# Kernel tuning notes

Measured on AMD Instinct MI355X. Metric: run time of the kernel, lower is better.

The kernel has to match this reference:

```python
import jax, jax.numpy as jnp
import numpy as np
from jax import lax

RATIOS = [0.5, 1.0, 2.0]
SCALES = [8, 16, 32]
BASE = 16
FEAT_STRIDE = 16
NMS_THRESH = 0.7
PRE_NMS = 2000
POST_NMS = 300
MIN_SIZE = 16.0
SCALE = 1.0
A = len(RATIOS) * len(SCALES)  # 9


def _anchor_base():
    ab = []
    py = px = BASE / 2.0
    for r in RATIOS:
        for s in SCALES:
            h = BASE * s * np.sqrt(r)
            w = BASE * s * np.sqrt(1.0 / r)
            ab.append([py - h / 2.0, px - w / 2.0, py + h / 2.0, px + w / 2.0])
    return jnp.asarray(np.array(ab, dtype=np.float32))  # (A,4)


def _shifted_anchors(H, W):
    base = _anchor_base()
    sy = jnp.arange(H, dtype=jnp.float32) * FEAT_STRIDE
    sx = jnp.arange(W, dtype=jnp.float32) * FEAT_STRIDE
    gy, gx = jnp.meshgrid(sy, sx, indexing='ij')
    shift = jnp.stack([gy.ravel(), gx.ravel(), gy.ravel(), gx.ravel()], axis=1)  # (K,4)
    return (shift[:, None, :] + base[None, :, :]).reshape(-1, 4)  # (K*A,4)


def _conv(x, w, b, pad):
    y = lax.conv_general_dilated(x, w, (1, 1), ((pad, pad), (pad, pad)),
                                 dimension_numbers=('NCHW', 'OIHW', 'NCHW'))
    return y + b[None, :, None, None]


def _loc2bbox(anchor, loc):
    h = anchor[:, 2] - anchor[:, 0]
    w = anchor[:, 3] - anchor[:, 1]
    cy = anchor[:, 0] + 0.5 * h
    cx = anchor[:, 1] + 0.5 * w
    dy, dx, dh, dw = loc[:, 0], loc[:, 1], loc[:, 2], loc[:, 3]
    ncy = dy * h + cy
    ncx = dx * w + cx
    nh = jnp.exp(dh) * h
    nw = jnp.exp(dw) * w
    return jnp.stack([ncy - 0.5 * nh, ncx - 0.5 * nw, ncy + 0.5 * nh, ncx + 0.5 * nw], axis=1)


def _iou_matrix(b):
    area = (b[:, 2] - b[:, 0]) * (b[:, 3] - b[:, 1])
    ty = jnp.maximum(b[:, None, 0], b[None, :, 0])
    tx = jnp.maximum(b[:, None, 1], b[None, :, 1])
    by = jnp.minimum(b[:, None, 2], b[None, :, 2])
    bx = jnp.minimum(b[:, None, 3], b[None, :, 3])
    inter = jnp.maximum(by - ty, 0.0) * jnp.maximum(bx - tx, 0.0)
    return inter / (area[:, None] + area[None, :] - inter)


def _proposals(loc_i, fg_i, anchor, img_h, img_w):
    boxes = _loc2bbox(anchor, loc_i)
    boxes = jnp.stack([
        jnp.clip(boxes[:, 0], 0.0, float(img_h)),
        jnp.clip(boxes[:, 1], 0.0, float(img_w)),
        jnp.clip(boxes[:, 2], 0.0, float(img_h)),
        jnp.clip(boxes[:, 3], 0.0, float(img_w)),
    ], axis=1)
    hs = boxes[:, 2] - boxes[:, 0]
    ws = boxes[:, 3] - boxes[:, 1]
    valid = (hs >= MIN_SIZE * SCALE) & (ws >= MIN_SIZE * SCALE)
    sc = jnp.where(valid, fg_i, -jnp.inf)
    top_sc, idx = lax.top_k(sc, PRE_NMS)          # sorted by score desc
    b = boxes[idx]                                # (PRE_NMS,4)
    iou = _iou_matrix(b)                          # (PRE_NMS,PRE_NMS)
    rng = jnp.arange(PRE_NMS)

    def body(i, keep):
        sup = (iou[i] > NMS_THRESH) & keep[i] & (rng > i)
        return keep & ~sup

    keep = lax.fori_loop(0, PRE_NMS, body, top_sc > -jnp.inf)
    order = jnp.argsort(jnp.where(keep, rng, PRE_NMS))  # kept indices first, score order
    sel = order[:POST_NMS]
    n_keep = jnp.sum(keep)
    valid_out = jnp.arange(POST_NMS) < n_keep
    rois = jnp.where(valid_out[:, None], b[sel], 0.0)
    return rois, valid_out


def setup_inputs() -> dict:
    key = jax.random.key(0)
    ks = jax.random.split(key, 4)
    return {
        'x': jax.random.normal(ks[0], (4, 1024, 64, 64), dtype=jnp.float32),
        'conv1_w': 0.01 * jax.random.normal(ks[1], (512, 1024, 3, 3), dtype=jnp.float32),
        'conv1_b': jnp.zeros((512,), dtype=jnp.float32),
        'score_w': 0.01 * jax.random.normal(ks[2], (18, 512, 1, 1), dtype=jnp.float32),
        'score_b': jnp.zeros((18,), dtype=jnp.float32),
        'loc_w': 0.01 * jax.random.normal(ks[3], (36, 512, 1, 1), dtype=jnp.float32),
        'loc_b': jnp.zeros((36,), dtype=jnp.float32),
        'img_h': 1024,
        'img_w': 1024,
    }


def reference(x, conv1_w, conv1_b, score_w, score_b, loc_w, loc_b, img_h, img_w):
    n, _, H, W = x.shape
    anchor = _shifted_anchors(H, W)                       # (HWA,4)
    mid = jax.nn.relu(_conv(x, conv1_w, conv1_b, 1))
    rpn_locs = _conv(mid, loc_w, loc_b, 0).transpose(0, 2, 3, 1).reshape(n, -1, 4)
    rpn_scores = _conv(mid, score_w, score_b, 0).transpose(0, 2, 3, 1)
    soft = jax.nn.softmax(rpn_scores.reshape(n, H, W, A, 2), axis=4)
    rpn_fg = soft[..., 1].reshape(n, -1)
    rpn_scores = rpn_scores.reshape(n, -1, 2)
    rois, valid = jax.vmap(lambda l, s: _proposals(l, s, anchor, img_h, img_w))(rpn_locs, rpn_fg)
    roi_indices = jnp.where(valid, jnp.arange(n, dtype=jnp.int32)[:, None], -1)
    return (rpn_locs, rpn_scores, rois.reshape(-1, 4), roi_indices.reshape(-1), anchor)
```

## Files before the change

### kernel.cpp

```cpp
#include <hip/hip_runtime.h>
#include <math.h>

#define NIMG 4
#define CIN 1024
#define CMID 512
#define HGT 64
#define WID 64
#define NA 9
#define NPOS 36864
#define PRE 2000
#define POST 300

#define LOCOFF   0
#define SCOREOFF 589824
#define ROISOFF  884736
#define RIDXOFF  889536
#define ANCHOFF  890736

__global__ __launch_bounds__(256) void wtrans_kernel(
    const float* __restrict__ w, float* __restrict__ wt)
{
    __shared__ float ts[64][65];
    const int t = threadIdx.x;
    const int rt0 = blockIdx.x * 64;
    const int ct0 = blockIdx.y * 64;
    const int j = t & 63;
    const int i0 = t >> 6;
#pragma unroll
    for (int k = 0; k < 16; ++k) {
        int i = i0 + k * 4;
        ts[i][j] = w[(size_t)(ct0 + i) * (CIN * 9) + rt0 + j];
    }
    __syncthreads();
#pragma unroll
    for (int k = 0; k < 16; ++k) {
        int jj = i0 + k * 4;
        wt[(size_t)(rt0 + jj) * CMID + ct0 + j] = ts[j][jj];
    }
}

__global__ __launch_bounds__(256) void conv1_kernel(
    const float* __restrict__ x, const float* __restrict__ wt,
    const float* __restrict__ bias, float* __restrict__ mid)
{
    __shared__ __align__(16) float  xs[8][6][68];
    __shared__ __align__(16) double wsh[8][9][32];
    const int t = threadIdx.x;
    const int rowgrp = blockIdx.x, coutgrp = blockIdx.y, img = blockIdx.z;
    const int r0 = rowgrp * 4, c0 = coutgrp * 32;
    const int pixgrp = t & 7, cgrp = (t >> 3) & 7, rowi = t >> 6;
    const int p0 = pixgrp * 8, cc0 = cgrp * 4;

    double acc[8][4];
#pragma unroll
    for (int i = 0; i < 8; ++i)
#pragma unroll
        for (int c = 0; c < 4; ++c) acc[i][c] = 0.0;

    for (int ci0 = 0; ci0 < CIN; ci0 += 8) {
        for (int idx = t; idx < 8 * 6 * 66; idx += 256) {
            int cin = idx / 396, rem = idx % 396;
            int row = rem / 66, col = rem % 66;
            int gr = r0 - 1 + row, gc = col - 1;
            float v = 0.f;
            if (gr >= 0 && gr < HGT && gc >= 0 && gc < WID)
                v = x[((img * CIN + ci0 + cin) * HGT + gr) * WID + gc];
            xs[cin][row][col] = v;
        }
        for (int idx = t; idx < 8 * 9 * 32; idx += 256) {
            int cout = idx & 31, r = idx >> 5;
            wsh[r / 9][r % 9][cout] =
                (double)wt[(size_t)((ci0 + r / 9) * 9 + r % 9) * CMID + c0 + cout];
        }
        __syncthreads();

#pragma unroll 1
        for (int cin = 0; cin < 8; ++cin) {
#pragma unroll
            for (int dy = 0; dy < 3; ++dy) {
                const float* xr = &xs[cin][rowi + dy][p0];
                float4 xa = *(const float4*)xr;
                float4 xb = *(const float4*)(xr + 4);
                float2 xc = *(const float2*)(xr + 8);
                double xd[10];
                xd[0] = (double)xa.x; xd[1] = (double)xa.y;
                xd[2] = (double)xa.z; xd[3] = (double)xa.w;
                xd[4] = (double)xb.x; xd[5] = (double)xb.y;
                xd[6] = (double)xb.z; xd[7] = (double)xb.w;
                xd[8] = (double)xc.x; xd[9] = (double)xc.y;
#pragma unroll
                for (int dx = 0; dx < 3; ++dx) {
                    const double* wp = &wsh[cin][dy * 3 + dx][cc0];
                    double2 wa = *(const double2*)(wp);
                    double2 wb = *(const double2*)(wp + 2);
                    double w0 = wa.x, w1 = wa.y, w2 = wb.x, w3 = wb.y;
#pragma unroll
                    for (int i = 0; i < 8; ++i) {
                        double xv = xd[i + dx];
                        acc[i][0] += xv * w0;
                        acc[i][1] += xv * w1;
                        acc[i][2] += xv * w2;
                        acc[i][3] += xv * w3;
                    }
                }
            }
        }
        __syncthreads();
    }

#pragma unroll
    for (int co = 0; co < 4; ++co) {
        double bb = (double)bias[c0 + cc0 + co];
        float tmp[8];
#pragma unroll
        for (int i = 0; i < 8; ++i) {
            double v = acc[i][co] + bb;
            v = v > 0.0 ? v : 0.0;
            tmp[i] = (float)v;
        }
        float* dst = &mid[((img * CMID + c0 + cc0 + co) * HGT + (r0 + rowi)) * WID + p0];
        *(float4*)dst = make_float4(tmp[0], tmp[1], tmp[2], tmp[3]);
        *(float4*)(dst + 4) = make_float4(tmp[4], tmp[5], tmp[6], tmp[7]);
    }
}

__global__ __launch_bounds__(256) void conv1x1_kernel(
    const float* __restrict__ mid,
    const float* __restrict__ sw, const float* __restrict__ sb,
    const float* __restrict__ lw, const float* __restrict__ lb,
    float* __restrict__ out, double* __restrict__ locws, double* __restrict__ keyws)
{
    const int t = threadIdx.x;
    const int p = blockIdx.x * 256 + t;
    const int g = blockIdx.y;
    const int img = blockIdx.z;

    double acc[14];
#pragma unroll
    for (int k = 0; k < 14; ++k) acc[k] = 0.0;

    const float* mp = &mid[(size_t)img * CMID * 4096 + p];
    for (int cin = 0; cin < CMID; ++cin) {
        double xd = (double)mp[(size_t)cin * 4096];
#pragma unroll
        for (int k = 0; k < 14; ++k) {
            int c = g * 14 + k;
            double wv = 0.0;
            if (c < 36)      wv = (double)lw[c * CMID + cin];
            else if (c < 54) wv = (double)sw[(c - 36) * CMID + cin];
            acc[k] += xd * wv;
        }
    }

    double prev = 0.0;
#pragma unroll
    for (int k = 0; k < 14; ++k) {
        int c = g * 14 + k;
        if (c >= 54) continue;
        if (c < 36) {
            double v = acc[k] + (double)lb[c];
            int a = c >> 2, cc = c & 3;
            size_t ix = (size_t)img * NPOS + (size_t)p * NA + a;
            locws[ix * 4 + cc] = v;
            out[LOCOFF + ix * 4 + cc] = (float)v;
        } else {
            int sc = c - 36;
            double v = acc[k] + (double)sb[sc];
            int a = sc >> 1;
            size_t ix = (size_t)img * NPOS + (size_t)p * NA + a;
            out[SCOREOFF + ix * 2 + (sc & 1)] = (float)v;
            if (sc & 1) keyws[ix] = v - prev;
            prev = v;
        }
    }
}

__device__ __forceinline__ unsigned mono_of(double k) {
    unsigned fb = __float_as_uint((float)k);
    return (fb & 0x80000000u) ? ~fb : (fb | 0x80000000u);
}

__global__ __launch_bounds__(256) void boxes_kernel(
    double* __restrict__ keyio, const double* __restrict__ locws,
    const int* __restrict__ imh, const int* __restrict__ imw,
    float* __restrict__ out, double* __restrict__ boxes, unsigned* __restrict__ hist)
{
    __shared__ unsigned lh[4096];
    const int t = threadIdx.x;
    const int img = blockIdx.y;
    const int pos = blockIdx.x * 256 + t;
    for (int i = t; i < 4096; i += 256) lh[i] = 0;
    __syncthreads();

    int a = pos % 9, hw = pos / 9;
    int hy = hw >> 6, hx = hw & 63;
    int r_idx = a / 3, s_idx = a % 3;
    double ratio = r_idx == 0 ? 0.5 : (r_idx == 1 ? 1.0 : 2.0);
    double scl   = s_idx == 0 ? 8.0 : (s_idx == 1 ? 16.0 : 32.0);
    double hh2 = 8.0 * scl * sqrt(ratio);
    double ww2 = 8.0 * scl * sqrt(1.0 / ratio);
    float ay1 = (float)(8.0 - hh2), ax1 = (float)(8.0 - ww2);
    float ay2 = (float)(8.0 + hh2), ax2 = (float)(8.0 + ww2);
    float sy = (float)(hy * 16), sx = (float)(hx * 16);
    float A0 = sy + ay1, A1 = sx + ax1, A2 = sy + ay2, A3 = sx + ax2;
    if (img == 0) {
        size_t ao = ANCHOFF + (size_t)pos * 4;
        out[ao + 0] = A0; out[ao + 1] = A1; out[ao + 2] = A2; out[ao + 3] = A3;
    }

    size_t ix = (size_t)img * NPOS + pos;
    const double* lp = &locws[ix * 4];
    double h = (double)A2 - (double)A0, w_ = (double)A3 - (double)A1;
    double cy = (double)A0 + 0.5 * h, cx = (double)A1 + 0.5 * w_;
    double dy = lp[0], dx = lp[1], dh = lp[2], dw = lp[3];
    double ncy = dy * h + cy, ncx = dx * w_ + cx;
    double nh = exp(dh) * h, nw = exp(dw) * w_;
    double Hc = (double)imh[0], Wc = (double)imw[0];
    double y1 = ncy - 0.5 * nh, x1 = ncx - 0.5 * nw;
    double y2 = ncy + 0.5 * nh, x2 = ncx + 0.5 * nw;
    y1 = fmin(fmax(y1, 0.0), Hc); x1 = fmin(fmax(x1, 0.0), Wc);
    y2 = fmin(fmax(y2, 0.0), Hc); x2 = fmin(fmax(x2, 0.0), Wc);
    boxes[ix * 4 + 0] = y1; boxes[ix * 4 + 1] = x1;
    boxes[ix * 4 + 2] = y2; boxes[ix * 4 + 3] = x2;

    bool valid = ((y2 - y1) >= 16.0) && ((x2 - x1) >= 16.0);
    double kg = valid ? keyio[ix] : -INFINITY;
    keyio[ix] = kg;
    atomicAdd(&lh[mono_of(kg) >> 20], 1u);
    __syncthreads();
    for (int i = t; i < 4096; i += 256)
        if (lh[i]) atomicAdd(&hist[img * 4096 + i], lh[i]);
}

__global__ void cutoff_kernel(const unsigned* __restrict__ hist, int* __restrict__ cutoffb)
{
    if (threadIdx.x) return;
    int img = blockIdx.x;
    unsigned cum = 0; int cb = 0;
    for (int b = 4095; b >= 0; --b) {
        cum += hist[img * 4096 + b];
        if (cum >= PRE) { cb = b; break; }
    }
    cutoffb[img] = cb;
}

__global__ __launch_bounds__(256) void compact_kernel(
    const double* __restrict__ keyio, const int* __restrict__ cutoffb,
    int* __restrict__ candCnt, int* __restrict__ candIdx, double* __restrict__ candKey)
{
    int img = blockIdx.y;
    int pos = blockIdx.x * 256 + threadIdx.x;
    size_t ix = (size_t)img * NPOS + pos;
    double k = keyio[ix];
    if ((int)(mono_of(k) >> 20) >= cutoffb[img]) {
        int p = atomicAdd(&candCnt[img], 1);
        candIdx[img * NPOS + p] = pos;
        candKey[(size_t)img * NPOS + p] = k;
    }
}

__global__ __launch_bounds__(256) void rank_kernel(
    const int* __restrict__ candCnt, const int* __restrict__ candIdx,
    const double* __restrict__ candKey, const double* __restrict__ boxes,
    int* __restrict__ topIdx, int* __restrict__ topValid, double* __restrict__ bsel)
{
    __shared__ double sk[256];
    __shared__ int si[256];
    int img = blockIdx.y, t = threadIdx.x;
    int M = candCnt[img];
    if (blockIdx.x * 256 >= M) return;
    int i = blockIdx.x * 256 + t;
    bool act = i < M;
    double ki = 0.0; int pi = 0;
    if (act) { ki = candKey[(size_t)img * NPOS + i]; pi = candIdx[img * NPOS + i]; }
    int rank = 0;
    for (int jb = 0; jb < M; jb += 256) {
        int j = jb + t;
        if (j < M) { sk[t] = candKey[(size_t)img * NPOS + j]; si[t] = candIdx[img * NPOS + j]; }
        __syncthreads();
        int lim = min(256, M - jb);
        if (act) {
            for (int jj = 0; jj < lim; ++jj) {
                double kj = sk[jj]; int pj = si[jj];
                rank += (kj > ki || (kj == ki && pj < pi)) ? 1 : 0;
            }
        }
        __syncthreads();
    }
    if (act && rank < PRE) {
        topIdx[img * PRE + rank] = pi;
        topValid[img * PRE + rank] = (ki != -INFINITY) ? 1 : 0;
        const double* bp = &boxes[((size_t)img * NPOS + pi) * 4];
        double* bs = &bsel[((size_t)img * PRE + rank) * 4];
        bs[0] = bp[0]; bs[1] = bp[1]; bs[2] = bp[2]; bs[3] = bp[3];
    }
}

__global__ __launch_bounds__(256) void mask_kernel(
    const double* __restrict__ bsel, unsigned long long* __restrict__ mask)
{
    int i = blockIdx.x, img = blockIdx.y, t = threadIdx.x;
    const double* bi = &bsel[((size_t)img * PRE + i) * 4];
    double y1i = bi[0], x1i = bi[1], y2i = bi[2], x2i = bi[3];
    double ai = (y2i - y1i) * (x2i - x1i);
#pragma unroll 1
    for (int it = 0; it < 8; ++it) {
        int j = it * 256 + t;
        bool pred = false;
        if (j < PRE && j > i) {
            const double* bj = &bsel[((size_t)img * PRE + j) * 4];
            double ty = fmax(y1i, bj[0]), tx = fmax(x1i, bj[1]);
            double by = fmin(y2i, bj[2]), bx = fmin(x2i, bj[3]);
            double inter = fmax(by - ty, 0.0) * fmax(bx - tx, 0.0);
            double aj = (bj[2] - bj[0]) * (bj[3] - bj[1]);
            double iou = inter / (ai + aj - inter);
            pred = iou > 0.7;
        }
        unsigned long long m = __ballot(pred);
        if ((t & 63) == 0)
            mask[((size_t)img * PRE + i) * 32 + it * 4 + (t >> 6)] = m;
    }
}

__global__ void nms_kernel(const unsigned long long* __restrict__ mask,
                           const int* __restrict__ topValid, int* __restrict__ keepA)
{
    int img = blockIdx.x, lane = threadIdx.x;
    size_t base = (size_t)img * PRE;
    unsigned long long remv = 0;
    if (lane < 32) {
        unsigned long long tv = 0;
        for (int b = 0; b < 64; ++b) {
            int idx = lane * 64 + b;
            if (idx < PRE && topValid[base + idx]) tv |= (1ull << b);
        }
        remv = ~tv;
    }
    const unsigned long long* mrow = &mask[base * 32];
    unsigned long long c0 = 0, c1 = 0, c2 = 0, c3 = 0;
    if (lane < 32) {
        c0 = mrow[(size_t)0 * 32 + lane]; c1 = mrow[(size_t)1 * 32 + lane];
        c2 = mrow[(size_t)2 * 32 + lane]; c3 = mrow[(size_t)3 * 32 + lane];
    }
    for (int i = 0; i < PRE; i += 4) {
        unsigned long long n0 = 0, n1 = 0, n2 = 0, n3 = 0;
        if (lane < 32 && i + 4 < PRE) {
            n0 = mrow[(size_t)(i + 4) * 32 + lane];
            n1 = mrow[(size_t)(i + 5) * 32 + lane];
            n2 = mrow[(size_t)(i + 6) * 32 + lane];
            n3 = mrow[(size_t)(i + 7) * 32 + lane];
        }
        {
            unsigned long long rw = __shfl(remv, i >> 6);
            int kp = !((rw >> (i & 63)) & 1ull);
            if (lane == 0) keepA[base + i] = kp;
            if (kp) remv |= c0;
        }
        {
            int ii = i + 1;
            unsigned long long rw = __shfl(remv, ii >> 6);
            int kp = !((rw >> (ii & 63)) & 1ull);
            if (lane == 0) keepA[base + ii] = kp;
            if (kp) remv |= c1;
        }
        {
            int ii = i + 2;
            unsigned long long rw = __shfl(remv, ii >> 6);
            int kp = !((rw >> (ii & 63)) & 1ull);
            if (lane == 0) keepA[base + ii] = kp;
            if (kp) remv |= c2;
        }
        {
            int ii = i + 3;
            unsigned long long rw = __shfl(remv, ii >> 6);
            int kp = !((rw >> (ii & 63)) & 1ull);
            if (lane == 0) keepA[base + ii] = kp;
            if (kp) remv |= c3;
        }
        c0 = n0; c1 = n1; c2 = n2; c3 = n3;
    }
}

__global__ __launch_bounds__(256) void final_kernel(
    const int* __restrict__ keepA, const double* __restrict__ bsel, float* __restrict__ out)
{
    __shared__ int ssum[256];
    __shared__ int stot;
    int img = blockIdx.x, t = threadIdx.x;
    size_t base = (size_t)img * PRE;
    int loc[8]; int s = 0;
#pragma unroll
    for (int k = 0; k < 8; ++k) {
        int i = t * 8 + k;
        loc[k] = (i < PRE) ? keepA[base + i] : 0;
        s += loc[k];
    }
    ssum[t] = s;
    __syncthreads();
    if (t == 0) {
        int run = 0;
        for (int u = 0; u < 256; ++u) { int tmp = ssum[u]; ssum[u] = run; run += tmp; }
        stot = run;
    }
    __syncthreads();
    int run = ssum[t];
#pragma unroll
    for (int k = 0; k < 8; ++k) {
        int i = t * 8 + k;
        if (i < PRE && loc[k]) {
            int p = run++;
            if (p < POST) {
                const double* bp = &bsel[(base + i) * 4];
                size_t ro = ROISOFF + ((size_t)img * POST + p) * 4;
                out[ro + 0] = (float)bp[0]; out[ro + 1] = (float)bp[1];
                out[ro + 2] = (float)bp[2]; out[ro + 3] = (float)bp[3];
                out[RIDXOFF + img * POST + p] = (float)img;
            }
        }
    }
    __syncthreads();
    int nk = stot;
    for (int r = t; r < POST; r += 256) {
        if (r >= nk) {
            size_t ro = ROISOFF + ((size_t)img * POST + r) * 4;
            out[ro + 0] = 0.f; out[ro + 1] = 0.f; out[ro + 2] = 0.f; out[ro + 3] = 0.f;
            out[RIDXOFF + img * POST + r] = -1.f;
        }
    }
}

extern "C" void kernel_launch(void* const* d_in, const int* in_sizes, int n_in,
                              void* d_out, int out_size, void* d_ws, size_t ws_size,
                              hipStream_t stream)
{
    const float* x   = (const float*)d_in[0];
    const float* c1w = (const float*)d_in[1];
    const float* c1b = (const float*)d_in[2];
    const float* sw  = (const float*)d_in[3];
    const float* sb  = (const float*)d_in[4];
    const float* lw  = (const float*)d_in[5];
    const float* lb  = (const float*)d_in[6];
    const int*   ih  = (const int*)d_in[7];
    const int*   iw  = (const int*)d_in[8];
    float* out = (float*)d_out;
    (void)in_sizes; (void)n_in; (void)out_size; (void)ws_size;

    char* ws = (char*)d_ws;
    size_t off = 0;
    auto alloc = [&](size_t bytes) -> void* {
        void* p = (void*)(ws + off);
        off = (off + bytes + 255) & ~(size_t)255;
        return p;
    };
    float*  mid      = (float*) alloc((size_t)NIMG * CMID * 4096 * 4);
    float*  wtr      = (float*) alloc((size_t)CMID * CIN * 9 * 4);
    double* locws    = (double*)alloc((size_t)NIMG * NPOS * 4 * 8);
    double* keyws    = (double*)alloc((size_t)NIMG * NPOS * 8);
    double* boxes    = (double*)alloc((size_t)NIMG * NPOS * 4 * 8);
    unsigned* hist   = (unsigned*)alloc((size_t)NIMG * 4096 * 4);
    int*    cutoffb  = (int*)   alloc(64);
    int*    candCnt  = (int*)   alloc(64);
    int*    candIdx  = (int*)   alloc((size_t)NIMG * NPOS * 4);
    double* candKey  = (double*)alloc((size_t)NIMG * NPOS * 8);
    int*    topIdx   = (int*)   alloc((size_t)NIMG * PRE * 4);
    int*    topValid = (int*)   alloc((size_t)NIMG * PRE * 4);
    double* bsel     = (double*)alloc((size_t)NIMG * PRE * 4 * 8);
    unsigned long long* mask = (unsigned long long*)alloc((size_t)NIMG * PRE * 32 * 8);
    int*    keepA    = (int*)   alloc((size_t)NIMG * PRE * 4);

    hipMemsetAsync(hist, 0, (size_t)NIMG * 4096 * 4, stream);
    hipMemsetAsync(candCnt, 0, 64, stream);

    wtrans_kernel <<<dim3(144, 8),       256, 0, stream>>>(c1w, wtr);
    conv1_kernel  <<<dim3(16, 16, NIMG), 256, 0, stream>>>(x, wtr, c1b, mid);
    conv1x1_kernel<<<dim3(16, 4, NIMG),  256, 0, stream>>>(mid, sw, sb, lw, lb, out, locws, keyws);
    boxes_kernel  <<<dim3(144, NIMG),    256, 0, stream>>>(keyws, locws, ih, iw, out, boxes, hist);
    cutoff_kernel <<<NIMG, 64, 0, stream>>>(hist, cutoffb);
    compact_kernel<<<dim3(144, NIMG),    256, 0, stream>>>(keyws, cutoffb, candCnt, candIdx, candKey);
    rank_kernel   <<<dim3(144, NIMG),    256, 0, stream>>>(candCnt, candIdx, candKey, boxes,
                                                           topIdx, topValid, bsel);
    mask_kernel   <<<dim3(PRE, NIMG),    256, 0, stream>>>(bsel, mask);
    nms_kernel    <<<NIMG, 64, 0, stream>>>(mask, topValid, keepA);
    final_kernel  <<<NIMG, 256, 0, stream>>>(keepA, bsel, out);
}
```

Before: 4.658 ms.

## Double-buffer conv1 loads via direct global-to-LDS with pre-converted fp64 weight slabs

The 3x3 conv now stages input rows and weights straight into LDS with global_load_lds, double-buffered so the next channel block loads while the current one computes. Only one barrier per iteration remains. Weights are pre-converted to double and laid out in contiguous per-cout-group slabs so they can be copied without conversion. Horizontal padding is handled in registers instead of being stored as halo columns. The cost is twice the weight workspace, a smaller channel block per stage, and correctness depends on the async LDS load semantics and the buffer-reuse ordering.

```diff
diff --git a/kernel.cpp b/kernel.cpp
--- a/kernel.cpp
+++ b/kernel.cpp
@@ -10,6 +10,7 @@
 #define NPOS 36864
 #define PRE 2000
 #define POST 300
+#define CBLK 4
 
 #define LOCOFF   0
 #define SCOREOFF 589824
@@ -17,8 +18,11 @@
 #define RIDXOFF  889536
 #define ANCHOFF  890736
 
+typedef __attribute__((address_space(1))) const void glob_cv;
+typedef __attribute__((address_space(3))) void lds_v;
+
 __global__ __launch_bounds__(256) void wtrans_kernel(
-    const float* __restrict__ w, float* __restrict__ wt)
+    const float* __restrict__ w, double* __restrict__ wt64)
 {
     __shared__ float ts[64][65];
     const int t = threadIdx.x;
@@ -32,24 +36,64 @@
         ts[i][j] = w[(size_t)(ct0 + i) * (CIN * 9) + rt0 + j];
     }
     __syncthreads();
+    const int cout = ct0 + j;
+    const size_t blk = (size_t)(cout >> 5) * (9216 * 32) + (cout & 31);
 #pragma unroll
     for (int k = 0; k < 16; ++k) {
         int jj = i0 + k * 4;
-        wt[(size_t)(rt0 + jj) * CMID + ct0 + j] = ts[j][jj];
+        wt64[blk + (size_t)(rt0 + jj) * 32] = (double)ts[j][jj];
     }
 }
 
 __global__ __launch_bounds__(256) void conv1_kernel(
-    const float* __restrict__ x, const float* __restrict__ wt,
+    const float* __restrict__ x, const double* __restrict__ wt64,
     const float* __restrict__ bias, float* __restrict__ mid)
 {
-    __shared__ __align__(16) float  xs[8][6][68];
-    __shared__ __align__(16) double wsh[8][9][32];
+    __shared__ __align__(16) float  Xl[2][CBLK][6][64];
+    __shared__ __align__(16) double Wl[2][CBLK][9][32];
     const int t = threadIdx.x;
     const int rowgrp = blockIdx.x, coutgrp = blockIdx.y, img = blockIdx.z;
-    const int r0 = rowgrp * 4, c0 = coutgrp * 32;
-    const int pixgrp = t & 7, cgrp = (t >> 3) & 7, rowi = t >> 6;
-    const int p0 = pixgrp * 8, cc0 = cgrp * 4;
+    const int y0 = rowgrp * 4, c0 = coutgrp * 32;
+    const int pg = t & 7, cg = (t >> 3) & 7, rowi = t >> 6;
+    const int p0 = pg * 8, cc0 = cg * 4;
+    const int lane = t & 63;
+
+    if (rowgrp == 0) {
+        for (int i = t; i < 2 * CBLK * 64; i += 256) {
+            int b = i / (CBLK * 64), rem = i % (CBLK * 64);
+            Xl[b][rem >> 6][0][rem & 63] = 0.f;
+        }
+    }
+    if (rowgrp == 15) {
+        for (int i = t; i < 2 * CBLK * 64; i += 256) {
+            int b = i / (CBLK * 64), rem = i % (CBLK * 64);
+            Xl[b][rem >> 6][5][rem & 63] = 0.f;
+        }
+    }
+
+    const int rlo = (rowgrp == 0) ? 1 : 0;
+    const int rhi = (rowgrp == 15) ? 4 : 5;
+    const int nrows = rhi - rlo + 1;
+    const double* wslab = wt64 + (size_t)coutgrp * (9216 * 32);
+
+    auto issue = [&](int ci0, int nb) {
+        int nx = CBLK * nrows;
+        for (int k = rowi; k < nx; k += 4) {
+            int cl = k / nrows, row = rlo + k % nrows;
+            int gr = y0 - 1 + row;
+            const float* gp =
+                &x[(((size_t)img * CIN + ci0 + cl) * HGT + gr) * WID] + lane;
+            __builtin_amdgcn_global_load_lds(
+                (glob_cv*)gp, (lds_v*)&Xl[nb][cl][row][0], 4, 0, 0);
+        }
+        const double* wb = wslab + (size_t)ci0 * (9 * 32);
+        double* ldsw = &Wl[nb][0][0][0];
+        for (int k = rowi; k < 9; k += 4) {
+            const double* gp = wb + k * 128 + lane * 2;
+            __builtin_amdgcn_global_load_lds(
+                (glob_cv*)gp, (lds_v*)(ldsw + k * 128), 16, 0, 0);
+        }
+    };
 
     double acc[8][4];
 #pragma unroll
@@ -57,43 +101,36 @@
 #pragma unroll
         for (int c = 0; c < 4; ++c) acc[i][c] = 0.0;
 
-    for (int ci0 = 0; ci0 < CIN; ci0 += 8) {
-        for (int idx = t; idx < 8 * 6 * 66; idx += 256) {
-            int cin = idx / 396, rem = idx % 396;
-            int row = rem / 66, col = rem % 66;
-            int gr = r0 - 1 + row, gc = col - 1;
-            float v = 0.f;
-            if (gr >= 0 && gr < HGT && gc >= 0 && gc < WID)
-                v = x[((img * CIN + ci0 + cin) * HGT + gr) * WID + gc];
-            xs[cin][row][col] = v;
-        }
-        for (int idx = t; idx < 8 * 9 * 32; idx += 256) {
-            int cout = idx & 31, r = idx >> 5;
-            wsh[r / 9][r % 9][cout] =
-                (double)wt[(size_t)((ci0 + r / 9) * 9 + r % 9) * CMID + c0 + cout];
-        }
+    issue(0, 0);
+
+#pragma unroll 1
+    for (int s = 0; s < 256; ++s) {
+        const int buf = s & 1;
         __syncthreads();
+        if (s < 255) issue((s + 1) * CBLK, buf ^ 1);
 
 #pragma unroll 1
-        for (int cin = 0; cin < 8; ++cin) {
+        for (int cl = 0; cl < CBLK; ++cl) {
 #pragma unroll
             for (int dy = 0; dy < 3; ++dy) {
-                const float* xr = &xs[cin][rowi + dy][p0];
-                float4 xa = *(const float4*)xr;
-                float4 xb = *(const float4*)(xr + 4);
-                float2 xc = *(const float2*)(xr + 8);
+                const float* xr = &Xl[buf][cl][rowi + dy][0];
+                float f0 = (pg != 0) ? xr[p0 - 1] : 0.f;
+                float4 xa = *(const float4*)(xr + p0);
+                float4 xb = *(const float4*)(xr + p0 + 4);
+                float f9 = (pg != 7) ? xr[p0 + 8] : 0.f;
                 double xd[10];
-                xd[0] = (double)xa.x; xd[1] = (double)xa.y;
-                xd[2] = (double)xa.z; xd[3] = (double)xa.w;
-                xd[4] = (double)xb.x; xd[5] = (double)xb.y;
-                xd[6] = (double)xb.z; xd[7] = (double)xb.w;
-                xd[8] = (double)xc.x; xd[9] = (double)xc.y;
+                xd[0] = (double)f0;
+                xd[1] = (double)xa.x; xd[2] = (double)xa.y;
+                xd[3] = (double)xa.z; xd[4] = (double)xa.w;
+                xd[5] = (double)xb.x; xd[6] = (double)xb.y;
+                xd[7] = (double)xb.z; xd[8] = (double)xb.w;
+                xd[9] = (double)f9;
 #pragma unroll
                 for (int dx = 0; dx < 3; ++dx) {
-                    const double* wp = &wsh[cin][dy * 3 + dx][cc0];
+                    const double* wp = &Wl[buf][cl][dy * 3 + dx][cc0];
                     double2 wa = *(const double2*)(wp);
-                    double2 wb = *(const double2*)(wp + 2);
-                    double w0 = wa.x, w1 = wa.y, w2 = wb.x, w3 = wb.y;
+                    double2 wb2 = *(const double2*)(wp + 2);
+                    double w0 = wa.x, w1 = wa.y, w2 = wb2.x, w3 = wb2.y;
 #pragma unroll
                     for (int i = 0; i < 8; ++i) {
                         double xv = xd[i + dx];
@@ -105,7 +142,6 @@
                 }
             }
         }
-        __syncthreads();
     }
 
 #pragma unroll
@@ -118,7 +154,7 @@
             v = v > 0.0 ? v : 0.0;
             tmp[i] = (float)v;
         }
-        float* dst = &mid[((img * CMID + c0 + cc0 + co) * HGT + (r0 + rowi)) * WID + p0];
+        float* dst = &mid[((img * CMID + c0 + cc0 + co) * HGT + (y0 + rowi)) * WID + p0];
         *(float4*)dst = make_float4(tmp[0], tmp[1], tmp[2], tmp[3]);
         *(float4*)(dst + 4) = make_float4(tmp[4], tmp[5], tmp[6], tmp[7]);
     }
@@ -453,7 +489,7 @@
         return p;
     };
     float*  mid      = (float*) alloc((size_t)NIMG * CMID * 4096 * 4);
-    float*  wtr      = (float*) alloc((size_t)CMID * CIN * 9 * 4);
+    double* wt64     = (double*)alloc((size_t)CMID * CIN * 9 * 8);
     double* locws    = (double*)alloc((size_t)NIMG * NPOS * 4 * 8);
     double* keyws    = (double*)alloc((size_t)NIMG * NPOS * 8);
     double* boxes    = (double*)alloc((size_t)NIMG * NPOS * 4 * 8);
@@ -471,8 +507,8 @@
     hipMemsetAsync(hist, 0, (size_t)NIMG * 4096 * 4, stream);
     hipMemsetAsync(candCnt, 0, 64, stream);
 
-    wtrans_kernel <<<dim3(144, 8),       256, 0, stream>>>(c1w, wtr);
-    conv1_kernel  <<<dim3(16, 16, NIMG), 256, 0, stream>>>(x, wtr, c1b, mid);
+    wtrans_kernel <<<dim3(144, 8),       256, 0, stream>>>(c1w, wt64);
+    conv1_kernel  <<<dim3(16, 16, NIMG), 256, 0, stream>>>(x, wt64, c1b, mid);
     conv1x1_kernel<<<dim3(16, 4, NIMG),  256, 0, stream>>>(mid, sw, sb, lw, lb, out, locws, keyws);
     boxes_kernel  <<<dim3(144, NIMG),    256, 0, stream>>>(keyws, locws, ih, iw, out, boxes, hist);
     cutoff_kernel <<<NIMG, 64, 0, stream>>>(hist, cutoffb);
```

New measurement: 4.715 ms. Within noise of the previous version (+1.2%).
